# Performance work log

Hardware: AMD Instinct MI355X
Metric: run time of the kernel (lower is better)

The kernel has to match this reference:

```python
import jax, jax.numpy as jnp
import numpy as np

B, S, D_IN, D_HID, D_OUT = 8, 2048, 1024, 1024, 1024


def setup_inputs() -> dict:
    key = jax.random.key(0)
    ks = jax.random.split(key, 11)
    def lin(kw, kb, fan_in, fan_out):
        bound = 1.0 / np.sqrt(fan_in)
        W = jax.random.uniform(kw, (fan_out, fan_in), minval=-bound, maxval=bound, dtype=jnp.float32)
        b = jax.random.uniform(kb, (fan_out,), minval=-bound, maxval=bound, dtype=jnp.float32)
        return W, b
    Wq, bq = lin(ks[0], ks[1], D_IN, D_HID)
    Wk, bk = lin(ks[2], ks[3], D_IN, D_HID)
    Wv, bv = lin(ks[4], ks[5], D_IN, D_HID)
    Wo, bo = lin(ks[6], ks[7], D_HID, D_OUT)
    gamma = jnp.ones((D_OUT,), jnp.float32)
    beta = jnp.zeros((D_OUT,), jnp.float32)
    x = jax.random.normal(ks[8], (B, S, D_IN), dtype=jnp.float32)
    return {"x": x, "Wq": Wq, "bq": bq, "Wk": Wk, "bk": bk,
            "Wv": Wv, "bv": bv, "Wo": Wo, "bo": bo,
            "gamma": gamma, "beta": beta}


def _layer_norm(x, gamma, beta, eps=1e-5):
    mu = jnp.mean(x, axis=-1, keepdims=True)
    var = jnp.var(x, axis=-1, keepdims=True)
    return (x - mu) * jax.lax.rsqrt(var + eps) * gamma + beta


def reference(x, Wq, bq, Wk, bk, Wv, bv, Wo, bo, gamma, beta):
    q = jnp.einsum('bsd,hd->bsh', x, Wq) + bq   # [B,S,H]
    k = jnp.einsum('bsd,hd->bsh', x, Wk) + bk
    v = jnp.einsum('bsd,hd->bsh', x, Wv) + bv
    scale = 1.0 / jnp.sqrt(jnp.float32(D_HID))
    scores = jnp.einsum('bqh,bkh->bqk', q, k) * scale  # [B,S,S]
    attn = jax.nn.softmax(scores, axis=-1)
    weighted = jnp.einsum('bqk,bkh->bqh', attn, v)     # [B,S,H]
    out = jnp.einsum('bsh,oh->bso', weighted, Wo) + bo # [B,S,O]
    return _layer_norm(out + x, gamma, beta)
```

## Files before the change

### kernel.cpp

```cpp
#include <hip/hip_runtime.h>
#include <hip/hip_bf16.h>
#include <math.h>


typedef __bf16 bf16;
typedef unsigned char u8;
typedef __attribute__((ext_vector_type(8))) __bf16 bf16x8;
typedef __attribute__((ext_vector_type(4))) __bf16 bf16x4;
typedef __attribute__((ext_vector_type(8))) int i32x8;
typedef __attribute__((ext_vector_type(16))) float f32x16;

__device__ __forceinline__ void async16(const u8* g, u8* l) {
    __builtin_amdgcn_global_load_lds(
        (const __attribute__((address_space(1))) void*)g,
        (__attribute__((address_space(3))) void*)l, 16, 0, 0);
}

#define WAITCNT_VM(n) __builtin_amdgcn_s_waitcnt((15 << 8) | (7 << 4) | (n))

__device__ __forceinline__ u8 to_fp8(float v) {
    return (u8)(__builtin_amdgcn_cvt_pk_fp8_f32(v, v, 0, 0) & 0xFF);
}

__global__ __launch_bounds__(256) void cast_f32_fp8(
    const float* __restrict__ in, u8* __restrict__ out, int n)
{
    int i = (blockIdx.x * 256 + threadIdx.x) * 8;
    if (i >= n) return;
    float4 a = *(const float4*)(in + i);
    float4 b = *(const float4*)(in + i + 4);
    int lo = __builtin_amdgcn_cvt_pk_fp8_f32(a.x, a.y, 0, 0);
    lo = __builtin_amdgcn_cvt_pk_fp8_f32(a.z, a.w, lo, 1);
    int hi = __builtin_amdgcn_cvt_pk_fp8_f32(b.x, b.y, 0, 0);
    hi = __builtin_amdgcn_cvt_pk_fp8_f32(b.z, b.w, hi, 1);
    int2 o = { lo, hi };
    *(int2*)(out + i) = o;
}

__global__ __launch_bounds__(256) void gemm_f8(
    const u8* __restrict__ A, long lda, long sA,
    const u8* __restrict__ B, long ldb, long sB,
    void* __restrict__ Cv, long ldc, long sC,
    const float* __restrict__ bias, int bias_mode,
    float scale, int c_mode, int K)
{
    __shared__ u8 lds[3][16384];

    const int gx = gridDim.x, gy = gridDim.y;
    const int slice = gx * gy;
    const int total = slice * gridDim.z;
    int flat = ((int)blockIdx.z * gy + (int)blockIdx.y) * gx + (int)blockIdx.x;
    if ((total & 7) == 0)
        flat = (flat & 7) * (total >> 3) + (flat >> 3);
    const int bz = flat / slice;
    const int rem = flat - bz * slice;
    const int by = rem / gx;
    const int bx = rem - by * gx;

    const int tid = threadIdx.x;
    const long tM = (long)by * 128;
    const long tN = (long)bx * 128;
    A += (long)bz * sA;
    B += (long)bz * sB;

    const int sline = tid >> 3;
    const int sch = (tid & 7) ^ (sline & 7);
    const int skb = (sch & 3) << 4;
    const int srofs = (sch & 4) << 4;
    const u8* gA0 = A + (tM + sline + srofs) * lda + skb;
    const u8* gA1 = gA0 + 32 * lda;
    const u8* gB0 = B + (tN + sline + srofs) * ldb + skb;
    const u8* gB1 = gB0 + 32 * ldb;
    const int dA0 = tid * 16,        dA1 = 4096 + tid * 16;
    const int dB0 = 8192 + tid * 16, dB1 = 12288 + tid * 16;

    const int w = tid >> 6, lane = tid & 63;
    const int wm = (w & 1) * 64, wn = (w >> 1) * 64;
    const int r32 = lane & 31, kh = lane >> 5;

    f32x16 acc[2][2] = {};

    const int iters = K >> 6;

    {
        u8* p = lds[0];
        async16(gA0, p + dA0); async16(gA1, p + dA1);
        async16(gB0, p + dB0); async16(gB1, p + dB1);
        u8* q = lds[1];
        async16(gA0 + 64, q + dA0); async16(gA1 + 64, q + dA1);
        async16(gB0 + 64, q + dB0); async16(gB1 + 64, q + dB1);
    }

    const int xr = r32 & 7;
    const int cbA = (w & 1) ? 4 : 0;
    const int cbB = (w >> 1) ? 4 : 0;
    const int oA0q0 = r32 * 128 + (((cbA + (kh << 1) + 0) ^ xr) << 4);
    const int oA0q1 = r32 * 128 + (((cbA + (kh << 1) + 1) ^ xr) << 4);
    const int oB0q0 = 8192 + r32 * 128 + (((cbB + (kh << 1) + 0) ^ xr) << 4);
    const int oB0q1 = 8192 + r32 * 128 + (((cbB + (kh << 1) + 1) ^ xr) << 4);

    int cur = 0;
    for (int it = 0; it < iters; ++it) {
        if (it + 1 < iters) WAITCNT_VM(4);
        else WAITCNT_VM(0);
        __builtin_amdgcn_s_barrier();

        if (it + 2 < iters) {
            int nb = cur + 2; if (nb >= 3) nb -= 3;
            u8* p = lds[nb];
            const long ko = (long)(it + 2) << 6;
            async16(gA0 + ko, p + dA0); async16(gA1 + ko, p + dA1);
            async16(gB0 + ko, p + dB0); async16(gB1 + ko, p + dB1);
        }

        const u8* cb = lds[cur];
        union F { i32x8 v; int4 q[2]; };
        F a0, a1, b0, b1;
        a0.q[0] = *(const int4*)&cb[oA0q0];
        a0.q[1] = *(const int4*)&cb[oA0q1];
        a1.q[0] = *(const int4*)&cb[oA0q0 + 4096];
        a1.q[1] = *(const int4*)&cb[oA0q1 + 4096];
        b0.q[0] = *(const int4*)&cb[oB0q0];
        b0.q[1] = *(const int4*)&cb[oB0q1];
        b1.q[0] = *(const int4*)&cb[oB0q0 + 4096];
        b1.q[1] = *(const int4*)&cb[oB0q1 + 4096];

        acc[0][0] = __builtin_amdgcn_mfma_scale_f32_32x32x64_f8f6f4(
            a0.v, b0.v, acc[0][0], 0, 0, 0, 0x7F7F7F7F, 0, 0x7F7F7F7F);
        acc[0][1] = __builtin_amdgcn_mfma_scale_f32_32x32x64_f8f6f4(
            a0.v, b1.v, acc[0][1], 0, 0, 0, 0x7F7F7F7F, 0, 0x7F7F7F7F);
        acc[1][0] = __builtin_amdgcn_mfma_scale_f32_32x32x64_f8f6f4(
            a1.v, b0.v, acc[1][0], 0, 0, 0, 0x7F7F7F7F, 0, 0x7F7F7F7F);
        acc[1][1] = __builtin_amdgcn_mfma_scale_f32_32x32x64_f8f6f4(
            a1.v, b1.v, acc[1][1], 0, 0, 0, 0x7F7F7F7F, 0, 0x7F7F7F7F);

        if (++cur >= 3) cur = 0;
    }

#pragma unroll
    for (int i = 0; i < 2; i++) {
#pragma unroll
        for (int j = 0; j < 2; j++) {
            const long gn = tN + wn + j * 32 + r32;
            const float bn = (bias_mode == 1) ? bias[gn] : 0.0f;
#pragma unroll
            for (int reg = 0; reg < 16; reg++) {
                const int rowf = (reg & 3) + 8 * (reg >> 2) + 4 * kh;
                const long gm = tM + wm + i * 32 + rowf;
                float v = acc[i][j][reg] * scale + bn;
                if (bias_mode == 2) v += bias[gm];
                if (c_mode == 0)
                    ((bf16*)Cv + (long)bz * sC)[gm * ldc + gn] = (bf16)v;
                else
                    ((u8*)Cv + (long)bz * sC)[gm * ldc + gn] = to_fp8(v);
            }
        }
    }
}

__global__ __launch_bounds__(256) void softmax_f8(
    const bf16* __restrict__ S, u8* __restrict__ P)
{
    const long row = blockIdx.x;
    const bf16* p = S + row * 2048;
    const int t = threadIdx.x;

    bf16x8 v = *(const bf16x8*)(p + t * 8);
    float f[8];
    float m = -3.0e38f;
#pragma unroll
    for (int i = 0; i < 8; i++) { f[i] = (float)v[i]; m = fmaxf(m, f[i]); }
    for (int o = 32; o; o >>= 1) m = fmaxf(m, __shfl_down(m, o));

    __shared__ float sm[4], ssum[4];
    if ((t & 63) == 0) sm[t >> 6] = m;
    __syncthreads();
    m = fmaxf(fmaxf(sm[0], sm[1]), fmaxf(sm[2], sm[3]));

    float s = 0.0f;
#pragma unroll
    for (int i = 0; i < 8; i++) { f[i] = __expf(f[i] - m); s += f[i]; }
    for (int o = 32; o; o >>= 1) s += __shfl_down(s, o);
    if ((t & 63) == 0) ssum[t >> 6] = s;
    __syncthreads();
    s = ssum[0] + ssum[1] + ssum[2] + ssum[3];

    const float c = 256.0f / s;
    int lo = __builtin_amdgcn_cvt_pk_fp8_f32(f[0] * c, f[1] * c, 0, 0);
    lo = __builtin_amdgcn_cvt_pk_fp8_f32(f[2] * c, f[3] * c, lo, 1);
    int hi = __builtin_amdgcn_cvt_pk_fp8_f32(f[4] * c, f[5] * c, 0, 0);
    hi = __builtin_amdgcn_cvt_pk_fp8_f32(f[6] * c, f[7] * c, hi, 1);
    int2 o = { lo, hi };
    *(int2*)(P + row * 2048 + t * 8) = o;
}

__global__ __launch_bounds__(256) void ln_res(
    const bf16* __restrict__ pre, const float* __restrict__ x,
    const float* __restrict__ gamma, const float* __restrict__ beta,
    float* __restrict__ out)
{
    const long row = blockIdx.x;
    const int t = threadIdx.x;
    const long base = row * 1024 + t * 4;

    bf16x4 a = *(const bf16x4*)(pre + base);
    float4 b = *(const float4*)(x + base);
    float v0 = (float)a[0] + b.x, v1 = (float)a[1] + b.y;
    float v2 = (float)a[2] + b.z, v3 = (float)a[3] + b.w;

    float s = v0 + v1 + v2 + v3;
    float q = v0 * v0 + v1 * v1 + v2 * v2 + v3 * v3;
    for (int o = 32; o; o >>= 1) { s += __shfl_down(s, o); q += __shfl_down(q, o); }

    __shared__ float ls[4], lq[4];
    if ((t & 63) == 0) { ls[t >> 6] = s; lq[t >> 6] = q; }
    __syncthreads();
    s = ls[0] + ls[1] + ls[2] + ls[3];
    q = lq[0] + lq[1] + lq[2] + lq[3];

    const float mean = s * (1.0f / 1024.0f);
    const float var = q * (1.0f / 1024.0f) - mean * mean;
    const float rstd = rsqrtf(var + 1e-5f);

    const int c = t * 4;
    float4 g = *(const float4*)(gamma + c);
    float4 be = *(const float4*)(beta + c);
    float4 o;
    o.x = (v0 - mean) * rstd * g.x + be.x;
    o.y = (v1 - mean) * rstd * g.y + be.y;
    o.z = (v2 - mean) * rstd * g.z + be.z;
    o.w = (v3 - mean) * rstd * g.w + be.w;
    *(float4*)(out + base) = o;
}

extern "C" void kernel_launch(void* const* d_in, const int* in_sizes, int n_in,
                              void* d_out, int out_size, void* d_ws, size_t ws_size,
                              hipStream_t stream)
{
    const float* x     = (const float*)d_in[0];
    const float* Wq    = (const float*)d_in[1];
    const float* bq    = (const float*)d_in[2];
    const float* Wk    = (const float*)d_in[3];
    const float* bk    = (const float*)d_in[4];
    const float* Wv    = (const float*)d_in[5];
    const float* bv    = (const float*)d_in[6];
    const float* Wo    = (const float*)d_in[7];
    const float* bo    = (const float*)d_in[8];
    const float* gamma = (const float*)d_in[9];
    const float* beta  = (const float*)d_in[10];
    float* out = (float*)d_out;

    char* ws = (char*)d_ws;
    u8* x8  = (u8*)(ws + (size_t)0);
    u8* Q8  = (u8*)(ws + (size_t)16777216);
    u8* K8  = (u8*)(ws + (size_t)33554432);
    u8* VT8 = (u8*)(ws + (size_t)50331648);
    u8* P8  = (u8*)(ws + (size_t)67108864);
    bf16* Sb = (bf16*)(ws + (size_t)104857600);
    u8* Wq8 = (u8*)(ws + (size_t)176160768);
    u8* Wk8 = Wq8 + 1048576;
    u8* Wv8 = Wk8 + 1048576;
    u8* Wo8 = Wv8 + 1048576;

    cast_f32_fp8<<<8192, 256, 0, stream>>>(x, x8, 16777216);
    cast_f32_fp8<<<512, 256, 0, stream>>>(Wq, Wq8, 1048576);
    cast_f32_fp8<<<512, 256, 0, stream>>>(Wk, Wk8, 1048576);
    cast_f32_fp8<<<512, 256, 0, stream>>>(Wv, Wv8, 1048576);
    cast_f32_fp8<<<512, 256, 0, stream>>>(Wo, Wo8, 1048576);

    gemm_f8<<<dim3(8, 128, 1), 256, 0, stream>>>(
        x8, 1024, 0, Wq8, 1024, 0, (void*)Q8, 1024, 0, bq, 1, 1.0f, 1, 1024);
    gemm_f8<<<dim3(8, 128, 1), 256, 0, stream>>>(
        x8, 1024, 0, Wk8, 1024, 0, (void*)K8, 1024, 0, bk, 1, 1.0f, 1, 1024);
    gemm_f8<<<dim3(128, 8, 1), 256, 0, stream>>>(
        Wv8, 1024, 0, x8, 1024, 0, (void*)VT8, 16384, 0, bv, 2, 1.0f, 1, 1024);
    gemm_f8<<<dim3(16, 16, 8), 256, 0, stream>>>(
        Q8, 1024, 2097152, K8, 1024, 2097152, (void*)Sb, 2048, 4194304,
        nullptr, 0, 0.03125f, 0, 1024);
    softmax_f8<<<16384, 256, 0, stream>>>(Sb, P8);
    gemm_f8<<<dim3(8, 16, 8), 256, 0, stream>>>(
        P8, 2048, 4194304, VT8, 16384, 2048, (void*)Q8, 1024, 2097152,
        nullptr, 0, 0.0625f, 1, 2048);
    gemm_f8<<<dim3(8, 128, 1), 256, 0, stream>>>(
        Q8, 1024, 0, Wo8, 1024, 0, (void*)Sb, 1024, 0, bo, 1, 0.0625f, 0, 1024);
    ln_res<<<16384, 256, 0, stream>>>((const bf16*)Sb, x, gamma, beta, out);
}
```

Baseline: 440.5 us.

## Enlarge GEMM tiles to 256x256 with 512 threads and interleave loads with MFMA

The fp8 GEMM tile grows from 128x128 to 256x256 with 8 waves per block. Each wave computes a 128x64 sub-tile, which raises data reuse per byte loaded into LDS. The main loop issues the next stage's async global-to-LDS loads between MFMA groups, with per-step barriers and setprio, to overlap memory and compute. The four weight-cast launches are merged into one kernel. The larger LDS footprint (96KB) and fewer blocks reduce occupancy and leave some GEMMs, such as the PV GEMM with 256 blocks, with fewer tiles to spread across CUs.

```diff
diff --git a/kernel.cpp b/kernel.cpp
--- a/kernel.cpp
+++ b/kernel.cpp
@@ -37,14 +37,34 @@
     *(int2*)(out + i) = o;
 }
 
-__global__ __launch_bounds__(256) void gemm_f8(
+__global__ __launch_bounds__(256) void cast_w4(
+    const float* __restrict__ W0, const float* __restrict__ W1,
+    const float* __restrict__ W2, const float* __restrict__ W3,
+    u8* __restrict__ out)
+{
+    const int b = blockIdx.x;
+    const int wsel = b >> 9;
+    const float* src = (wsel == 0) ? W0 : (wsel == 1) ? W1
+                     : (wsel == 2) ? W2 : W3;
+    const int i = ((b & 511) * 256 + threadIdx.x) * 8;
+    float4 a = *(const float4*)(src + i);
+    float4 c = *(const float4*)(src + i + 4);
+    int lo = __builtin_amdgcn_cvt_pk_fp8_f32(a.x, a.y, 0, 0);
+    lo = __builtin_amdgcn_cvt_pk_fp8_f32(a.z, a.w, lo, 1);
+    int hi = __builtin_amdgcn_cvt_pk_fp8_f32(c.x, c.y, 0, 0);
+    hi = __builtin_amdgcn_cvt_pk_fp8_f32(c.z, c.w, hi, 1);
+    int2 o = { lo, hi };
+    *(int2*)(out + (size_t)wsel * 1048576 + i) = o;
+}
+
+__global__ __launch_bounds__(512) void gemm_f8(
     const u8* __restrict__ A, long lda, long sA,
     const u8* __restrict__ B, long ldb, long sB,
     void* __restrict__ Cv, long ldc, long sC,
     const float* __restrict__ bias, int bias_mode,
     float scale, int c_mode, int K)
 {
-    __shared__ u8 lds[3][16384];
+    __shared__ u8 lds[3][32768];
 
     const int gx = gridDim.x, gy = gridDim.y;
     const int slice = gx * gy;
@@ -58,96 +78,109 @@
     const int bx = rem - by * gx;
 
     const int tid = threadIdx.x;
-    const long tM = (long)by * 128;
-    const long tN = (long)bx * 128;
+    const long tM = (long)by * 256;
+    const long tN = (long)bx * 256;
     A += (long)bz * sA;
     B += (long)bz * sB;
 
-    const int sline = tid >> 3;
-    const int sch = (tid & 7) ^ (sline & 7);
+    const int s = tid & 255;
+    const int line0 = s >> 3;
+    const int sch = (s & 7) ^ (line0 & 7);
     const int skb = (sch & 3) << 4;
-    const int srofs = (sch & 4) << 4;
-    const u8* gA0 = A + (tM + sline + srofs) * lda + skb;
-    const u8* gA1 = gA0 + 32 * lda;
-    const u8* gB0 = B + (tN + sline + srofs) * ldb + skb;
-    const u8* gB1 = gB0 + 32 * ldb;
-    const int dA0 = tid * 16,        dA1 = 4096 + tid * 16;
-    const int dB0 = 8192 + tid * 16, dB1 = 12288 + tid * 16;
+    const int srofs = (sch & 4) ? 128 : 0;
+    const u8* gsrc;
+    long gstr;
+    if (tid < 256) { gsrc = A + (tM + line0 + srofs) * lda + skb; gstr = lda; }
+    else           { gsrc = B + (tN + line0 + srofs) * ldb + skb; gstr = ldb; }
+    const int dbase = ((tid < 256) ? 0 : 16384) + s * 16;
 
     const int w = tid >> 6, lane = tid & 63;
-    const int wm = (w & 1) * 64, wn = (w >> 1) * 64;
+    const int wr = w >> 2, wc = w & 3;
     const int r32 = lane & 31, kh = lane >> 5;
-
-    f32x16 acc[2][2] = {};
-
-    const int iters = K >> 6;
-
-    {
-        u8* p = lds[0];
-        async16(gA0, p + dA0); async16(gA1, p + dA1);
-        async16(gB0, p + dB0); async16(gB1, p + dB1);
-        u8* q = lds[1];
-        async16(gA0 + 64, q + dA0); async16(gA1 + 64, q + dA1);
-        async16(gB0 + 64, q + dB0); async16(gB1 + 64, q + dB1);
+    const int xr = r32 & 7;
+
+    int oA[4][2], oB[2][2];
+    const int cbA = wr * 4;
+    const int cbB = (wc >> 1) * 4;
+#pragma unroll
+    for (int q = 0; q < 4; q++) {
+        const int lineA = q * 32 + r32;
+        oA[q][0] = lineA * 128 + (((cbA + 2 * kh + 0) ^ xr) << 4);
+        oA[q][1] = lineA * 128 + (((cbA + 2 * kh + 1) ^ xr) << 4);
     }
-
-    const int xr = r32 & 7;
-    const int cbA = (w & 1) ? 4 : 0;
-    const int cbB = (w >> 1) ? 4 : 0;
-    const int oA0q0 = r32 * 128 + (((cbA + (kh << 1) + 0) ^ xr) << 4);
-    const int oA0q1 = r32 * 128 + (((cbA + (kh << 1) + 1) ^ xr) << 4);
-    const int oB0q0 = 8192 + r32 * 128 + (((cbB + (kh << 1) + 0) ^ xr) << 4);
-    const int oB0q1 = 8192 + r32 * 128 + (((cbB + (kh << 1) + 1) ^ xr) << 4);
+#pragma unroll
+    for (int n = 0; n < 2; n++) {
+        const int lineB = (wc & 1) * 64 + n * 32 + r32;
+        oB[n][0] = 16384 + lineB * 128 + (((cbB + 2 * kh + 0) ^ xr) << 4);
+        oB[n][1] = 16384 + lineB * 128 + (((cbB + 2 * kh + 1) ^ xr) << 4);
+    }
+
+    f32x16 acc[4][2] = {};
+
+    const int T = K >> 6;
+
+#pragma unroll
+    for (int j = 0; j < 4; j++)
+        async16(gsrc + (long)j * 32 * gstr, &lds[0][dbase + j * 4096]);
+#pragma unroll
+    for (int j = 0; j < 4; j++)
+        async16(gsrc + 64 + (long)j * 32 * gstr, &lds[1][dbase + j * 4096]);
+    WAITCNT_VM(4);
+    __builtin_amdgcn_s_barrier();
+
+    union F { i32x8 v; int4 q2[2]; };
 
     int cur = 0;
-    for (int it = 0; it < iters; ++it) {
-        if (it + 1 < iters) WAITCNT_VM(4);
-        else WAITCNT_VM(0);
-        __builtin_amdgcn_s_barrier();
-
-        if (it + 2 < iters) {
-            int nb = cur + 2; if (nb >= 3) nb -= 3;
-            u8* p = lds[nb];
-            const long ko = (long)(it + 2) << 6;
-            async16(gA0 + ko, p + dA0); async16(gA1 + ko, p + dA1);
-            async16(gB0 + ko, p + dB0); async16(gB1 + ko, p + dB1);
+    for (int t = 0; t < T; ++t) {
+        const u8* cb = lds[cur];
+        int nb = cur + 2; if (nb >= 3) nb -= 3;
+        u8* pn = lds[nb];
+        const long ko = (long)(t + 2) << 6;
+        const bool pf = (t + 2 < T);
+
+        F b0, b1;
+#pragma unroll
+        for (int q = 0; q < 4; q++) {
+            if (pf) async16(gsrc + ko + (long)q * 32 * gstr,
+                            pn + dbase + q * 4096);
+            F aq;
+            aq.q2[0] = *(const int4*)&cb[oA[q][0]];
+            aq.q2[1] = *(const int4*)&cb[oA[q][1]];
+            if (q == 0) {
+                b0.q2[0] = *(const int4*)&cb[oB[0][0]];
+                b0.q2[1] = *(const int4*)&cb[oB[0][1]];
+                b1.q2[0] = *(const int4*)&cb[oB[1][0]];
+                b1.q2[1] = *(const int4*)&cb[oB[1][1]];
+            }
+            __builtin_amdgcn_s_barrier();
+            asm volatile("s_waitcnt lgkmcnt(0)" ::: "memory");
+            __builtin_amdgcn_s_setprio(1);
+            acc[q][0] = __builtin_amdgcn_mfma_scale_f32_32x32x64_f8f6f4(
+                aq.v, b0.v, acc[q][0], 0, 0, 0, 0x7F7F7F7F, 0, 0x7F7F7F7F);
+            acc[q][1] = __builtin_amdgcn_mfma_scale_f32_32x32x64_f8f6f4(
+                aq.v, b1.v, acc[q][1], 0, 0, 0, 0x7F7F7F7F, 0, 0x7F7F7F7F);
+            __builtin_amdgcn_s_setprio(0);
+            if (q == 3) {
+                if (pf) WAITCNT_VM(4);
+                else if (t + 1 < T) WAITCNT_VM(0);
+            }
+            __builtin_amdgcn_s_barrier();
         }
-
-        const u8* cb = lds[cur];
-        union F { i32x8 v; int4 q[2]; };
-        F a0, a1, b0, b1;
-        a0.q[0] = *(const int4*)&cb[oA0q0];
-        a0.q[1] = *(const int4*)&cb[oA0q1];
-        a1.q[0] = *(const int4*)&cb[oA0q0 + 4096];
-        a1.q[1] = *(const int4*)&cb[oA0q1 + 4096];
-        b0.q[0] = *(const int4*)&cb[oB0q0];
-        b0.q[1] = *(const int4*)&cb[oB0q1];
-        b1.q[0] = *(const int4*)&cb[oB0q0 + 4096];
-        b1.q[1] = *(const int4*)&cb[oB0q1 + 4096];
-
-        acc[0][0] = __builtin_amdgcn_mfma_scale_f32_32x32x64_f8f6f4(
-            a0.v, b0.v, acc[0][0], 0, 0, 0, 0x7F7F7F7F, 0, 0x7F7F7F7F);
-        acc[0][1] = __builtin_amdgcn_mfma_scale_f32_32x32x64_f8f6f4(
-            a0.v, b1.v, acc[0][1], 0, 0, 0, 0x7F7F7F7F, 0, 0x7F7F7F7F);
-        acc[1][0] = __builtin_amdgcn_mfma_scale_f32_32x32x64_f8f6f4(
-            a1.v, b0.v, acc[1][0], 0, 0, 0, 0x7F7F7F7F, 0, 0x7F7F7F7F);
-        acc[1][1] = __builtin_amdgcn_mfma_scale_f32_32x32x64_f8f6f4(
-            a1.v, b1.v, acc[1][1], 0, 0, 0, 0x7F7F7F7F, 0, 0x7F7F7F7F);
 
         if (++cur >= 3) cur = 0;
     }
 
 #pragma unroll
-    for (int i = 0; i < 2; i++) {
-#pragma unroll
-        for (int j = 0; j < 2; j++) {
-            const long gn = tN + wn + j * 32 + r32;
+    for (int q = 0; q < 4; q++) {
+#pragma unroll
+        for (int n = 0; n < 2; n++) {
+            const long gn = tN + wc * 64 + n * 32 + r32;
             const float bn = (bias_mode == 1) ? bias[gn] : 0.0f;
 #pragma unroll
             for (int reg = 0; reg < 16; reg++) {
                 const int rowf = (reg & 3) + 8 * (reg >> 2) + 4 * kh;
-                const long gm = tM + wm + i * 32 + rowf;
-                float v = acc[i][j][reg] * scale + bn;
+                const long gm = tM + wr * 128 + q * 32 + rowf;
+                float v = acc[q][n][reg] * scale + bn;
                 if (bias_mode == 2) v += bias[gm];
                 if (c_mode == 0)
                     ((bf16*)Cv + (long)bz * sC)[gm * ldc + gn] = (bf16)v;
@@ -258,30 +291,27 @@
     u8* P8  = (u8*)(ws + (size_t)67108864);
     bf16* Sb = (bf16*)(ws + (size_t)104857600);
     u8* Wq8 = (u8*)(ws + (size_t)176160768);
+
+    cast_f32_fp8<<<8192, 256, 0, stream>>>(x, x8, 16777216);
+    cast_w4<<<2048, 256, 0, stream>>>(Wq, Wk, Wv, Wo, Wq8);
     u8* Wk8 = Wq8 + 1048576;
     u8* Wv8 = Wk8 + 1048576;
     u8* Wo8 = Wv8 + 1048576;
 
-    cast_f32_fp8<<<8192, 256, 0, stream>>>(x, x8, 16777216);
-    cast_f32_fp8<<<512, 256, 0, stream>>>(Wq, Wq8, 1048576);
-    cast_f32_fp8<<<512, 256, 0, stream>>>(Wk, Wk8, 1048576);
-    cast_f32_fp8<<<512, 256, 0, stream>>>(Wv, Wv8, 1048576);
-    cast_f32_fp8<<<512, 256, 0, stream>>>(Wo, Wo8, 1048576);
-
-    gemm_f8<<<dim3(8, 128, 1), 256, 0, stream>>>(
+    gemm_f8<<<dim3(4, 64, 1), 512, 0, stream>>>(
         x8, 1024, 0, Wq8, 1024, 0, (void*)Q8, 1024, 0, bq, 1, 1.0f, 1, 1024);
-    gemm_f8<<<dim3(8, 128, 1), 256, 0, stream>>>(
+    gemm_f8<<<dim3(4, 64, 1), 512, 0, stream>>>(
         x8, 1024, 0, Wk8, 1024, 0, (void*)K8, 1024, 0, bk, 1, 1.0f, 1, 1024);
-    gemm_f8<<<dim3(128, 8, 1), 256, 0, stream>>>(
+    gemm_f8<<<dim3(64, 4, 1), 512, 0, stream>>>(
         Wv8, 1024, 0, x8, 1024, 0, (void*)VT8, 16384, 0, bv, 2, 1.0f, 1, 1024);
-    gemm_f8<<<dim3(16, 16, 8), 256, 0, stream>>>(
+    gemm_f8<<<dim3(8, 8, 8), 512, 0, stream>>>(
         Q8, 1024, 2097152, K8, 1024, 2097152, (void*)Sb, 2048, 4194304,
         nullptr, 0, 0.03125f, 0, 1024);
     softmax_f8<<<16384, 256, 0, stream>>>(Sb, P8);
-    gemm_f8<<<dim3(8, 16, 8), 256, 0, stream>>>(
+    gemm_f8<<<dim3(4, 8, 8), 512, 0, stream>>>(
         P8, 2048, 4194304, VT8, 16384, 2048, (void*)Q8, 1024, 2097152,
         nullptr, 0, 0.0625f, 1, 2048);
-    gemm_f8<<<dim3(8, 128, 1), 256, 0, stream>>>(
+    gemm_f8<<<dim3(4, 64, 1), 512, 0, stream>>>(
         Q8, 1024, 0, Wo8, 1024, 0, (void*)Sb, 1024, 0, bo, 1, 0.0625f, 0, 1024);
     ln_res<<<16384, 256, 0, stream>>>((const bf16*)Sb, x, gamma, beta, out);
 }
```

After: 489.7 us. 11.2% more time.
